# Kernel tuning notes

Hardware: AMD Instinct MI355X
Metric: run time of the kernel (lower is better)

The kernel has to match this reference:

```python
import jax, jax.numpy as jnp
import numpy as np

RCUT, RCUT_SMTH = 6.0, 0.5
SEL = [32, 64]
SEC = [0, 32, 96]
PAIRS = [(0, 0), (0, 1), (1, 1)]  # (ti, tj) with ti <= tj, matching stacked weight index
NF, NLOC, NALL = 1, 256, 512
NNEI = sum(SEL)
NG = 96


def setup_inputs() -> dict:
    key = jax.random.key(0)
    ks = jax.random.split(key, 10)
    # coords in a 4A cube so most neighbor distances are inside rcut=6
    extended_coord = jax.random.uniform(ks[0], (NF, NALL * 3), dtype=jnp.float32) * 4.0
    nl = jax.random.randint(ks[1], (NF, NLOC, NNEI), 0, NALL - 1)
    # shift indices >= own local index by 1 to avoid self-neighbors (zero distance)
    nlist = nl + (nl >= jnp.arange(NLOC)[None, :, None]).astype(nl.dtype)
    extended_atype = jax.random.randint(ks[2], (NF, NALL), 0, 2)
    mean = jnp.zeros((2, NNEI, 4), jnp.float32)
    stddev = jnp.ones((2, NNEI, 4), jnp.float32)
    def w(k, shape, fan):
        return jax.random.normal(k, shape, jnp.float32) / np.float32(np.sqrt(fan))
    W1 = w(ks[3], (3, 1, 24), 1.0)
    b1 = 0.1 * jax.random.normal(ks[4], (3, 24), jnp.float32)
    W2 = w(ks[5], (3, 24, 48), 24.0)
    b2 = 0.1 * jax.random.normal(ks[6], (3, 48), jnp.float32)
    W3 = w(ks[7], (3, 48, 96), 48.0)
    b3 = 0.1 * jax.random.normal(ks[8], (3, 96), jnp.float32)
    return dict(nlist=nlist, extended_coord=extended_coord, extended_atype=extended_atype,
                mean=mean, stddev=stddev, W1=W1, b1=b1, W2=W2, b2=b2, W3=W3, b3=b3)


def _smooth_weight(r, rmin, rmax):
    uu = (r - rmin) / (rmax - rmin)
    vv = uu * uu * uu * (-6.0 * uu * uu + 15.0 * uu - 10.0) + 1.0
    return jnp.where(r <= rmin, 1.0, jnp.where(r >= rmax, 0.0, vv))


def _env_mat(nlist, coord, atype, mean, stddev):
    nf, nloc, nnei = nlist.shape
    coord = coord.reshape(nf, -1, 3)
    mask = nlist >= 0
    nl = jnp.where(mask, nlist, 0)
    # gather neighbor coords: nf x nloc x nnei x 3
    coord_r = jnp.take_along_axis(coord, nl.reshape(nf, -1, 1), axis=1).reshape(nf, nloc, nnei, 3)
    diff = coord_r - coord[:, :nloc, None, :]
    length = jnp.linalg.norm(diff, axis=-1, keepdims=True)
    length = length + (~mask)[..., None].astype(diff.dtype)  # avoid 0-div on padded entries
    t0 = 1.0 / length
    t1 = diff / (length * length)
    sw = _smooth_weight(length, RCUT_SMTH, RCUT) * mask[..., None].astype(diff.dtype)
    env = jnp.concatenate([t0, t1], axis=-1) * sw  # nf x nloc x nnei x 4
    loc_type = atype[:, :nloc]
    dmatrix = (env - mean[loc_type]) / stddev[loc_type]
    return dmatrix, sw


def _embed(x, W1, b1, W2, b2, W3, b3):
    # EmbeddingNet 1->24->48->96, tanh, resnet doubling residuals
    h1 = jnp.tanh(x @ W1 + b1)
    h2 = jnp.tanh(h1 @ W2 + b2) + jnp.concatenate([h1, h1], axis=-1)
    h3 = jnp.tanh(h2 @ W3 + b3) + jnp.concatenate([h2, h2], axis=-1)
    return h3


def reference(nlist, extended_coord, extended_atype, mean, stddev, W1, b1, W2, b2, W3, b3):
    nf, nloc, nnei = nlist.shape
    dmatrix, sw = _env_mat(nlist, extended_coord, extended_atype, mean, stddev)
    dm = dmatrix.reshape(nf * nloc, nnei, 4)
    result = jnp.zeros((nf * nloc, NG), dm.dtype)
    for p, (ti, tj) in enumerate(PAIRS):
        rr_i = dm[:, SEC[ti]:SEC[ti + 1], 1:]  # nfnl x nt_i x 3
        rr_j = dm[:, SEC[tj]:SEC[tj + 1], 1:]  # nfnl x nt_j x 3
        env_ij = jnp.einsum('ijm,ikm->ijk', rr_i, rr_j)  # nfnl x nt_i x nt_j
        gg = _embed(env_ij[..., None], W1[p], b1[p], W2[p], b2[p], W3[p], b3[p])
        res_ij = jnp.einsum('ijk,ijkm->im', env_ij, gg)
        result = result + res_ij * (1.0 / (SEL[ti] * SEL[tj]))
    return result.reshape(nf, nloc, NG)
```

## Files before the change

kernel.cpp:

```cpp
#include <hip/hip_runtime.h>

#define NLOC 256
#define NNEI 96
#define NG   96
#define S2LE 2.88539008177793f

typedef __attribute__((ext_vector_type(8))) short short8;
typedef __attribute__((ext_vector_type(4))) float f32x4;
union Frag { uint4 u; short8 s; };

__device__ __forceinline__ float tanh_sc(float s) {
    float e = __builtin_amdgcn_exp2f(s);
    return 1.0f - 2.0f * __builtin_amdgcn_rcpf(e + 1.0f);
}
__device__ __forceinline__ unsigned short f2bf(float f) {
    unsigned int u = __float_as_uint(f);
    u += 0x7FFFu + ((u >> 16) & 1u);
    return (unsigned short)(u >> 16);
}
__device__ __forceinline__ unsigned short f2bf_rhu(float f) {
    return (unsigned short)((__float_as_uint(f) + 0x8000u) >> 16);
}
__device__ __forceinline__ unsigned int pack_bf2(float lo, float hi) {
    unsigned int a = __float_as_uint(lo) + 0x8000u;
    unsigned int b = __float_as_uint(hi) + 0x8000u;
    return __builtin_amdgcn_perm(b, a, 0x07060302);
}
__device__ __forceinline__ void wave_fence() {
    asm volatile("s_waitcnt lgkmcnt(0)" ::: "memory");
    __builtin_amdgcn_sched_barrier(0);
}

__global__ __launch_bounds__(256) void prep_kernel(
        const float* __restrict__ W1, const float* __restrict__ b1,
        const float* __restrict__ W2, const float* __restrict__ b2,
        const float* __restrict__ W3, const float* __restrict__ b3,
        unsigned short* __restrict__ wf2, unsigned short* __restrict__ wf3,
        unsigned short* __restrict__ wfJ,
        float* __restrict__ w1s, float* __restrict__ b1s,
        float* __restrict__ b2s, float* __restrict__ b3s,
        const int* __restrict__ nlist, const float* __restrict__ coord,
        const int* __restrict__ atype,
        const float* __restrict__ mean, const float* __restrict__ stddev,
        float4* __restrict__ rrle) {
    if (blockIdx.x >= 15) {
        if (rrle == nullptr) return;
        int t = (blockIdx.x - 15) * 256 + threadIdx.x;
        int i = t / 96, n = t - i * 96;
        int idx = nlist[i * NNEI + n];
        bool msk = idx >= 0;
        int safe = msk ? idx : 0;
        float cx = coord[i*3], cy = coord[i*3+1], cz = coord[i*3+2];
        float dx = coord[safe*3]   - cx;
        float dy = coord[safe*3+1] - cy;
        float dz = coord[safe*3+2] - cz;
        float rn = sqrtf(dx*dx + dy*dy + dz*dz) + (msk ? 0.0f : 1.0f);
        float sw;
        if (rn <= 0.5f)      sw = 1.0f;
        else if (rn >= 6.0f) sw = 0.0f;
        else {
            float uu = (rn - 0.5f) * (1.0f / 5.5f);
            sw = uu*uu*uu*(uu*(-6.0f*uu + 15.0f) - 10.0f) + 1.0f;
        }
        if (!msk) sw = 0.0f;
        float ir2 = 1.0f / (rn * rn);
        int ty = atype[i];
        const float* mu = mean   + (ty * NNEI + n) * 4;
        const float* sd = stddev + (ty * NNEI + n) * 4;
        float vx = (dx * ir2 * sw - mu[1]) / sd[1];
        float vy = (dy * ir2 * sw - mu[2]) / sd[2];
        float vz = (dz * ir2 * sw - mu[3]) / sd[3];
        rrle[t] = make_float4(vx, vy, vz, 0.0f);
        return;
    }
    int t = blockIdx.x * blockDim.x + threadIdx.x;
    if (t < 2880) {
        int p = t / 960;
        int r = t % 960;
        int tile = r / 64;
        int l = r % 64;
        int nlo = l & 15, g = l >> 4;
        short8 v;
        if (tile < 3) {
            int nt = tile;
            #pragma unroll
            for (int j = 0; j < 8; j++) {
                int k = g * 8 + j;
                float w = (k < 24) ? W2[(p * 24 + k) * 48 + nt * 16 + nlo] * S2LE : 0.0f;
                v[j] = (short)f2bf(w);
            }
            *(short8*)(wf2 + ((p * 3 + nt) * 64 + l) * 8) = v;
        } else {
            int tt = tile - 3;
            int nt = tt >> 1, kc = tt & 1;
            #pragma unroll
            for (int j = 0; j < 8; j++) {
                int kk = (kc == 0) ? (g * 8 + j) : ((j < 4) ? (32 + g * 4 + j) : -1);
                float w = (kk >= 0) ? W3[(p * 48 + kk) * 96 + nt * 16 + nlo] * S2LE : 0.0f;
                v[j] = (short)f2bf(w);
            }
            *(short8*)(wf3 + ((p * 12 + nt * 2 + kc) * 64 + l) * 8) = v;
        }
    } else if (t < 3264) {
        int t2 = t - 2880;
        int f = t2 >> 6, l = t2 & 63;
        int ml = l & 15, g = l >> 4;
        short8 v;
        if (f < 3) {
            int c24 = (f * 16 + ml) % 24;
            #pragma unroll
            for (int j = 0; j < 8; j++)
                v[j] = (short)((g * 8 + j == c24) ? 0x3F80 : 0);
        } else {
            int nt2 = f - 3;
            if (nt2 < 2) {
                int c = nt2 * 16 + ml;
                #pragma unroll
                for (int j = 0; j < 8; j++)
                    v[j] = (short)((g * 8 + j == c) ? 0x3F80 : 0);
            } else {
                #pragma unroll
                for (int j = 0; j < 8; j++)
                    v[j] = (short)((j < 4 && (g * 4 + j) == ml) ? 0x3F80 : 0);
            }
        }
        *(short8*)(wfJ + (f * 64 + l) * 8) = v;
    } else if (t < 3768) {
        int u = t - 3264;
        if (u < 72)       { w1s[u] = W1[u] * S2LE; b1s[u] = b1[u] * S2LE; }
        else if (u < 216) { b2s[u - 72]  = b2[u - 72]  * S2LE; }
        else              { b3s[u - 216] = b3[u - 216] * S2LE; }
    }
}

template<bool GR>
__launch_bounds__(256)
__global__ void mlp_kernel(const int* __restrict__ nlist, const float* __restrict__ coord,
                           const int* __restrict__ atype,
                           const float* __restrict__ mean, const float* __restrict__ stddev,
                           const float* __restrict__ w1s, const float* __restrict__ b1s,
                           const float* __restrict__ b2s, const float* __restrict__ b3s,
                           const unsigned short* __restrict__ wf2,
                           const unsigned short* __restrict__ wf3,
                           const unsigned short* __restrict__ wfJ,
                           const float4* __restrict__ rrle,
                           float* __restrict__ out) {
    __shared__ __align__(16) unsigned char smem[40448];
    unsigned short* h1s = (unsigned short*)smem;
    unsigned short* h2s = (unsigned short*)(smem + 12288);
    float*          resf = (float*)(smem + 38912);
    unsigned char*  h2b = smem + 12288;

    int tid = threadIdx.x;
    int blk = blockIdx.x;
    int i = blk / 20;
    int b = blk - i * 20;

    int p, base_e, offi, offj, count, Aint;
    float scale;
    bool tri;
    if (b < 3)       { p=0; base_e=b*256;      offi=0;  offj=0;  scale=1.0f/1024.0f; count=528;  tri=true;  Aint=65;  }
    else if (b < 11) { p=1; base_e=(b-3)*256;  offi=0;  offj=32; scale=1.0f/2048.0f; count=2048; tri=false; Aint=0;   }
    else             { p=2; base_e=(b-11)*256; offi=32; offj=32; scale=1.0f/4096.0f; count=2080; tri=true;  Aint=129; }

    int l  = tid & 63;
    int w  = tid >> 6;
    int ml = l & 15, g = l >> 4;

    if (!GR) {
        if (tid < NNEI) {
            int n = tid;
            int idx = nlist[i * NNEI + n];
            bool msk = idx >= 0;
            int safe = msk ? idx : 0;
            float cx = coord[i*3], cy = coord[i*3+1], cz = coord[i*3+2];
            float dx = coord[safe*3]   - cx;
            float dy = coord[safe*3+1] - cy;
            float dz = coord[safe*3+2] - cz;
            float rn = sqrtf(dx*dx + dy*dy + dz*dz) + (msk ? 0.0f : 1.0f);
            float sw;
            if (rn <= 0.5f)      sw = 1.0f;
            else if (rn >= 6.0f) sw = 0.0f;
            else {
                float uu = (rn - 0.5f) * (1.0f / 5.5f);
                sw = uu*uu*uu*(uu*(-6.0f*uu + 15.0f) - 10.0f) + 1.0f;
            }
            if (!msk) sw = 0.0f;
            float ir2 = 1.0f / (rn * rn);
            int ty = atype[i];
            const float* mu = mean   + (ty * NNEI + n) * 4;
            const float* sd = stddev + (ty * NNEI + n) * 4;
            float vx = (dx * ir2 * sw - mu[1]) / sd[1];
            float vy = (dy * ir2 * sw - mu[2]) / sd[2];
            float vz = (dz * ir2 * sw - mu[3]) / sd[3];
            float* hp = (float*)(h2b + (96 + n) * 104 + 96);
            hp[0] = vx; hp[1] = vy;
            *(float*)(h2b + (192 + (n >> 1)) * 104 + 96 + ((n & 1) << 2)) = vz;
        }
        __syncthreads();
    }

    float xs;
    {
        int e = base_e + tid;
        bool valid = e < count;
        int ec = valid ? e : 0;
        int jj, kk;
        float mult = 1.0f;
        if (!tri) { jj = ec >> 6; kk = ec & 63; }
        else {
            float Af = (float)Aint;
            int j = (int)((Af - sqrtf(Af*Af - 8.0f*(float)ec)) * 0.5f);
            int Tj1 = ((j+1)*(Aint-j-1)) >> 1;
            if (ec >= Tj1) j++;
            int Tj = (j*(Aint-j)) >> 1;
            if (ec < Tj) { j--; Tj = (j*(Aint-j)) >> 1; }
            jj = j; kk = j + (ec - Tj);
            mult = (jj == kk) ? 1.0f : 2.0f;
        }
        int ja = offi + jj, kb = offj + kk;
        float x;
        if (GR) {
            float4 ra = rrle[i * NNEI + ja];
            float4 rb = rrle[i * NNEI + kb];
            x = ra.x*rb.x + ra.y*rb.y + ra.z*rb.z;
        } else {
            const float* pa = (const float*)(h2b + (96 + ja) * 104 + 96);
            const float* pb = (const float*)(h2b + (96 + kb) * 104 + 96);
            float az = *(const float*)(h2b + (192 + (ja >> 1)) * 104 + 96 + ((ja & 1) << 2));
            float bz = *(const float*)(h2b + (192 + (kb >> 1)) * 104 + 96 + ((kb & 1) << 2));
            x = pa[0]*pb[0] + pa[1]*pb[1] + az*bz;
        }
        x = valid ? x : 0.0f;
        xs = x * mult * scale;

        const float* w1 = w1s + p * 24;
        const float* c1 = b1s + p * 24;
        float h1v[24];
        #pragma unroll
        for (int u = 0; u < 24; u++)
            h1v[u] = tanh_sc(fmaf(x, w1[u], c1[u]));
        #pragma unroll
        for (int t8 = 0; t8 < 3; t8++) {
            uint4 q = make_uint4(pack_bf2(h1v[8*t8+0], h1v[8*t8+1]),
                                 pack_bf2(h1v[8*t8+2], h1v[8*t8+3]),
                                 pack_bf2(h1v[8*t8+4], h1v[8*t8+5]),
                                 pack_bf2(h1v[8*t8+6], h1v[8*t8+7]));
            *(uint4*)(h1s + tid*24 + 8*t8) = q;
        }
    }
    wave_fence();

    short8 bw2[3], jf2[3];
    float  b2c[3];
    #pragma unroll
    for (int nt = 0; nt < 3; nt++) {
        bw2[nt] = *(const short8*)(wf2 + ((p*3 + nt)*64 + l)*8);
        jf2[nt] = *(const short8*)(wfJ + (nt*64 + l)*8);
        b2c[nt] = b2s[p*48 + nt*16 + ml];
    }
    f32x4 ones = {1.f, 1.f, 1.f, 1.f};
    int aoff = (g == 3) ? 0 : g * 8;
    #pragma unroll
    for (int mi = 0; mi < 4; mi++) {
        int mt = w*4 + mi;
        int arow = mt*16 + ml;
        uint2 lo = *(const uint2*)(h1s + arow*24 + aoff);
        uint2 hi = *(const uint2*)(h1s + arow*24 + aoff + 4);
        Frag fa; fa.u = make_uint4(lo.x, lo.y, hi.x, hi.y);
        #pragma unroll
        for (int nt = 0; nt < 3; nt++) {
            f32x4 bini = {b2c[nt], b2c[nt], b2c[nt], b2c[nt]};
            f32x4 acc = __builtin_amdgcn_mfma_f32_16x16x32_bf16(fa.s, bw2[nt], bini, 0, 0, 0);
            f32x4 aj  = __builtin_amdgcn_mfma_f32_16x16x32_bf16(fa.s, jf2[nt], ones, 0, 0, 0);
            int col = nt*16 + ml;
            #pragma unroll
            for (int r = 0; r < 4; r++) {
                int orow = mt*16 + g*4 + r;
                float e2 = __builtin_amdgcn_exp2f(acc[r]);
                float rc = __builtin_amdgcn_rcpf(e2 + 1.0f);
                float v  = fmaf(-2.0f, rc, aj[r]);
                h2s[orow*52 + col] = f2bf_rhu(v);
            }
        }
    }
    wave_fence();

    short8 a3a[4], a3b[4];
    float  xv[4][4];
    #pragma unroll
    for (int mi = 0; mi < 4; mi++) {
        int mt = w*4 + mi;
        int arow = mt*16 + ml;
        uint2 lo = *(const uint2*)(h2s + arow*52 + g*8);
        uint2 hi = *(const uint2*)(h2s + arow*52 + g*8 + 4);
        Frag fa; fa.u = make_uint4(lo.x, lo.y, hi.x, hi.y);
        a3a[mi] = fa.s;
        uint2 t2 = *(const uint2*)(h2s + arow*52 + 32 + g*4);
        Frag fb; fb.u = make_uint4(t2.x, t2.y, 0u, 0u);
        a3b[mi] = fb.s;
        int xb = (l & 48) + mi * 64;
        #pragma unroll
        for (int r = 0; r < 4; r++)
            xv[mi][r] = __int_as_float(
                __builtin_amdgcn_ds_bpermute(xb + r*4, __float_as_int(xs)));
    }
    short8 jf3[3];
    #pragma unroll
    for (int q = 0; q < 3; q++)
        jf3[q] = *(const short8*)(wfJ + ((3 + q)*64 + l)*8);

    #pragma unroll
    for (int nt2 = 0; nt2 < 3; nt2++) {
        f32x4 ajp[4];
        #pragma unroll
        for (int mi = 0; mi < 4; mi++)
            ajp[mi] = __builtin_amdgcn_mfma_f32_16x16x32_bf16(
                (nt2 == 2) ? a3b[mi] : a3a[mi], jf3[nt2], ones, 0, 0, 0);
        #pragma unroll
        for (int h = 0; h < 2; h++) {
            int nt = nt2 + 3*h;
            short8 b30 = *(const short8*)(wf3 + ((p*12 + nt*2 + 0)*64 + l)*8);
            short8 b31 = *(const short8*)(wf3 + ((p*12 + nt*2 + 1)*64 + l)*8);
            float b3c = b3s[p*96 + nt*16 + ml];
            float facc = 0.0f;
            #pragma unroll
            for (int mi = 0; mi < 4; mi++) {
                f32x4 bini = {b3c, b3c, b3c, b3c};
                f32x4 acc = __builtin_amdgcn_mfma_f32_16x16x32_bf16(a3a[mi], b30, bini, 0, 0, 0);
                acc = __builtin_amdgcn_mfma_f32_16x16x32_bf16(a3b[mi], b31, acc, 0, 0, 0);
                #pragma unroll
                for (int r = 0; r < 4; r++) {
                    float e2 = __builtin_amdgcn_exp2f(acc[r]);
                    float rc = __builtin_amdgcn_rcpf(e2 + 1.0f);
                    float h3 = fmaf(-2.0f, rc, ajp[mi][r]);
                    facc = fmaf(xv[mi][r], h3, facc);
                }
            }
            facc += __shfl_xor(facc, 16, 64);
            facc += __shfl_xor(facc, 32, 64);
            if (l < 16) resf[w*96 + nt*16 + ml] = facc;
        }
    }
    __syncthreads();
    if (tid < NG) {
        float s = resf[tid] + resf[96 + tid] + resf[192 + tid] + resf[288 + tid];
        atomicAdd(&out[i*NG + tid], s);
    }
}

extern "C" void kernel_launch(void* const* d_in, const int* in_sizes, int n_in,
                              void* d_out, int out_size, void* d_ws, size_t ws_size,
                              hipStream_t stream) {
    const int*   nlist  = (const int*)  d_in[0];
    const float* coord  = (const float*)d_in[1];
    const int*   atype  = (const int*)  d_in[2];
    const float* mean   = (const float*)d_in[3];
    const float* stddev = (const float*)d_in[4];
    const float* W1     = (const float*)d_in[5];
    const float* b1     = (const float*)d_in[6];
    const float* W2     = (const float*)d_in[7];
    const float* b2     = (const float*)d_in[8];
    const float* W3     = (const float*)d_in[9];
    const float* b3     = (const float*)d_in[10];
    float* out = (float*)d_out;

    char* ws = (char*)d_ws;
    unsigned short* wf2 = (unsigned short*)(ws + 0);
    unsigned short* wf3 = (unsigned short*)(ws + 9216);
    unsigned short* wfJ = (unsigned short*)(ws + 46080);
    float* w1s = (float*)(ws + 52224);
    float* b1s = (float*)(ws + 52512);
    float* b2s = (float*)(ws + 52800);
    float* b3s = (float*)(ws + 53376);
    size_t need = 55296 + (size_t)NLOC * NNEI * 16;
    bool gr = ws_size >= need;
    float4* rrle = gr ? (float4*)(ws + 55296) : nullptr;

    prep_kernel<<<gr ? 111 : 15, 256, 0, stream>>>(
        W1, b1, W2, b2, W3, b3, wf2, wf3, wfJ, w1s, b1s, b2s, b3s,
        nlist, coord, atype, mean, stddev, rrle);
    if (gr)
        mlp_kernel<true><<<NLOC * 20, 256, 0, stream>>>(
            nlist, coord, atype, mean, stddev,
            w1s, b1s, b2s, b3s, wf2, wf3, wfJ, rrle, out);
    else
        mlp_kernel<false><<<NLOC * 20, 256, 0, stream>>>(
            nlist, coord, atype, mean, stddev,
            w1s, b1s, b2s, b3s, wf2, wf3, wfJ, rrle, out);
}
```

Measured before the change: 135.2 us.

## Process layer-2/3 in two row chunks to shrink shared memory footprint

Splits each wave's four M-tiles into two chunks of two, computing the layer-2 output into a smaller per-chunk shared buffer and consuming it immediately in layer 3 while accumulating partial sums in registers. This cuts LDS usage per block from about 40KB to 27KB so more blocks can be resident per CU, and reduces live fragment registers. The env-matrix staging moves into the result buffer, which needs an extra block barrier in the non-GR path. The cost is more loop overhead, more wave fences and an extra sync.

```diff
diff --git a/kernel.cpp b/kernel.cpp
--- a/kernel.cpp
+++ b/kernel.cpp
@@ -145,11 +145,11 @@
                            const unsigned short* __restrict__ wfJ,
                            const float4* __restrict__ rrle,
                            float* __restrict__ out) {
-    __shared__ __align__(16) unsigned char smem[40448];
-    unsigned short* h1s = (unsigned short*)smem;
-    unsigned short* h2s = (unsigned short*)(smem + 12288);
-    float*          resf = (float*)(smem + 38912);
-    unsigned char*  h2b = smem + 12288;
+    __shared__ __align__(16) unsigned char smem[27136];
+    unsigned short* h1s  = (unsigned short*)smem;
+    unsigned char*  h1b  = smem;
+    unsigned char*  h2c  = smem + 12288;
+    float*          resf = (float*)(smem + 25600);
 
     int tid = threadIdx.x;
     int blk = blockIdx.x;
@@ -190,12 +190,9 @@
             int ty = atype[i];
             const float* mu = mean   + (ty * NNEI + n) * 4;
             const float* sd = stddev + (ty * NNEI + n) * 4;
-            float vx = (dx * ir2 * sw - mu[1]) / sd[1];
-            float vy = (dy * ir2 * sw - mu[2]) / sd[2];
-            float vz = (dz * ir2 * sw - mu[3]) / sd[3];
-            float* hp = (float*)(h2b + (96 + n) * 104 + 96);
-            hp[0] = vx; hp[1] = vy;
-            *(float*)(h2b + (192 + (n >> 1)) * 104 + 96 + ((n & 1) << 2)) = vz;
+            resf[n*3+0] = (dx * ir2 * sw - mu[1]) / sd[1];
+            resf[n*3+1] = (dy * ir2 * sw - mu[2]) / sd[2];
+            resf[n*3+2] = (dz * ir2 * sw - mu[3]) / sd[3];
         }
         __syncthreads();
     }
@@ -225,11 +222,8 @@
             float4 rb = rrle[i * NNEI + kb];
             x = ra.x*rb.x + ra.y*rb.y + ra.z*rb.z;
         } else {
-            const float* pa = (const float*)(h2b + (96 + ja) * 104 + 96);
-            const float* pb = (const float*)(h2b + (96 + kb) * 104 + 96);
-            float az = *(const float*)(h2b + (192 + (ja >> 1)) * 104 + 96 + ((ja & 1) << 2));
-            float bz = *(const float*)(h2b + (192 + (kb >> 1)) * 104 + 96 + ((kb & 1) << 2));
-            x = pa[0]*pb[0] + pa[1]*pb[1] + az*bz;
+            x = resf[ja*3+0]*resf[kb*3+0] + resf[ja*3+1]*resf[kb*3+1]
+              + resf[ja*3+2]*resf[kb*3+2];
         }
         x = valid ? x : 0.0f;
         xs = x * mult * scale;
@@ -246,101 +240,117 @@
                                  pack_bf2(h1v[8*t8+2], h1v[8*t8+3]),
                                  pack_bf2(h1v[8*t8+4], h1v[8*t8+5]),
                                  pack_bf2(h1v[8*t8+6], h1v[8*t8+7]));
-            *(uint4*)(h1s + tid*24 + 8*t8) = q;
+            *(uint4*)(h1b + tid*48 + 16*t8) = q;
         }
     }
     wave_fence();
-
-    short8 bw2[3], jf2[3];
-    float  b2c[3];
+    if (!GR) __syncthreads();
+
+    short8 bw2[3], jf2[3], jf3[3];
+    float  b2c[3], b3c6[6];
     #pragma unroll
     for (int nt = 0; nt < 3; nt++) {
         bw2[nt] = *(const short8*)(wf2 + ((p*3 + nt)*64 + l)*8);
         jf2[nt] = *(const short8*)(wfJ + (nt*64 + l)*8);
+        jf3[nt] = *(const short8*)(wfJ + ((3 + nt)*64 + l)*8);
         b2c[nt] = b2s[p*48 + nt*16 + ml];
     }
+    #pragma unroll
+    for (int q = 0; q < 6; q++) {
+        int nt = (q >> 1) + 3 * (q & 1);
+        b3c6[q] = b3s[p*96 + nt*16 + ml];
+    }
     f32x4 ones = {1.f, 1.f, 1.f, 1.f};
-    int aoff = (g == 3) ? 0 : g * 8;
+    int aoffB = (g == 3) ? 0 : g * 16;
+    float facc[6] = {0.f, 0.f, 0.f, 0.f, 0.f, 0.f};
+
     #pragma unroll
-    for (int mi = 0; mi < 4; mi++) {
-        int mt = w*4 + mi;
-        int arow = mt*16 + ml;
-        uint2 lo = *(const uint2*)(h1s + arow*24 + aoff);
-        uint2 hi = *(const uint2*)(h1s + arow*24 + aoff + 4);
-        Frag fa; fa.u = make_uint4(lo.x, lo.y, hi.x, hi.y);
+    for (int c = 0; c < 2; c++) {
         #pragma unroll
-        for (int nt = 0; nt < 3; nt++) {
-            f32x4 bini = {b2c[nt], b2c[nt], b2c[nt], b2c[nt]};
-            f32x4 acc = __builtin_amdgcn_mfma_f32_16x16x32_bf16(fa.s, bw2[nt], bini, 0, 0, 0);
-            f32x4 aj  = __builtin_amdgcn_mfma_f32_16x16x32_bf16(fa.s, jf2[nt], ones, 0, 0, 0);
-            int col = nt*16 + ml;
-            #pragma unroll
-            for (int r = 0; r < 4; r++) {
-                int orow = mt*16 + g*4 + r;
-                float e2 = __builtin_amdgcn_exp2f(acc[r]);
-                float rc = __builtin_amdgcn_rcpf(e2 + 1.0f);
-                float v  = fmaf(-2.0f, rc, aj[r]);
-                h2s[orow*52 + col] = f2bf_rhu(v);
-            }
-        }
-    }
-    wave_fence();
-
-    short8 a3a[4], a3b[4];
-    float  xv[4][4];
-    #pragma unroll
-    for (int mi = 0; mi < 4; mi++) {
-        int mt = w*4 + mi;
-        int arow = mt*16 + ml;
-        uint2 lo = *(const uint2*)(h2s + arow*52 + g*8);
-        uint2 hi = *(const uint2*)(h2s + arow*52 + g*8 + 4);
-        Frag fa; fa.u = make_uint4(lo.x, lo.y, hi.x, hi.y);
-        a3a[mi] = fa.s;
-        uint2 t2 = *(const uint2*)(h2s + arow*52 + 32 + g*4);
-        Frag fb; fb.u = make_uint4(t2.x, t2.y, 0u, 0u);
-        a3b[mi] = fb.s;
-        int xb = (l & 48) + mi * 64;
-        #pragma unroll
-        for (int r = 0; r < 4; r++)
-            xv[mi][r] = __int_as_float(
-                __builtin_amdgcn_ds_bpermute(xb + r*4, __float_as_int(xs)));
-    }
-    short8 jf3[3];
-    #pragma unroll
-    for (int q = 0; q < 3; q++)
-        jf3[q] = *(const short8*)(wfJ + ((3 + q)*64 + l)*8);
-
-    #pragma unroll
-    for (int nt2 = 0; nt2 < 3; nt2++) {
-        f32x4 ajp[4];
-        #pragma unroll
-        for (int mi = 0; mi < 4; mi++)
-            ajp[mi] = __builtin_amdgcn_mfma_f32_16x16x32_bf16(
-                (nt2 == 2) ? a3b[mi] : a3a[mi], jf3[nt2], ones, 0, 0, 0);
-        #pragma unroll
-        for (int h = 0; h < 2; h++) {
-            int nt = nt2 + 3*h;
-            short8 b30 = *(const short8*)(wf3 + ((p*12 + nt*2 + 0)*64 + l)*8);
-            short8 b31 = *(const short8*)(wf3 + ((p*12 + nt*2 + 1)*64 + l)*8);
-            float b3c = b3s[p*96 + nt*16 + ml];
-            float facc = 0.0f;
-            #pragma unroll
-            for (int mi = 0; mi < 4; mi++) {
-                f32x4 bini = {b3c, b3c, b3c, b3c};
-                f32x4 acc = __builtin_amdgcn_mfma_f32_16x16x32_bf16(a3a[mi], b30, bini, 0, 0, 0);
-                acc = __builtin_amdgcn_mfma_f32_16x16x32_bf16(a3b[mi], b31, acc, 0, 0, 0);
+        for (int m01 = 0; m01 < 2; m01++) {
+            int mi2 = c*2 + m01;
+            int mt = w*4 + mi2;
+            int arow = mt*16 + ml;
+            uint2 lo = *(const uint2*)(h1b + arow*48 + aoffB);
+            uint2 hi = *(const uint2*)(h1b + arow*48 + aoffB + 8);
+            Frag fa; fa.u = make_uint4(lo.x, lo.y, hi.x, hi.y);
+            int lbase = w*32 + m01*16 + g*4;
+            #pragma unroll
+            for (int nt = 0; nt < 3; nt++) {
+                f32x4 bini = {b2c[nt], b2c[nt], b2c[nt], b2c[nt]};
+                f32x4 acc = __builtin_amdgcn_mfma_f32_16x16x32_bf16(fa.s, bw2[nt], bini, 0, 0, 0);
+                f32x4 aj  = __builtin_amdgcn_mfma_f32_16x16x32_bf16(fa.s, jf2[nt], ones, 0, 0, 0);
+                int col = nt*16 + ml;
                 #pragma unroll
                 for (int r = 0; r < 4; r++) {
                     float e2 = __builtin_amdgcn_exp2f(acc[r]);
                     float rc = __builtin_amdgcn_rcpf(e2 + 1.0f);
-                    float h3 = fmaf(-2.0f, rc, ajp[mi][r]);
-                    facc = fmaf(xv[mi][r], h3, facc);
+                    float v  = fmaf(-2.0f, rc, aj[r]);
+                    *(unsigned short*)(h2c + (lbase + r)*104 + col*2) = f2bf_rhu(v);
                 }
             }
-            facc += __shfl_xor(facc, 16, 64);
-            facc += __shfl_xor(facc, 32, 64);
-            if (l < 16) resf[w*96 + nt*16 + ml] = facc;
-        }
+        }
+        wave_fence();
+
+        short8 a3a[2], a3b[2];
+        float  xv[2][4];
+        #pragma unroll
+        for (int m01 = 0; m01 < 2; m01++) {
+            int mi2 = c*2 + m01;
+            int lrow = w*32 + m01*16 + ml;
+            uint2 lo = *(const uint2*)(h2c + lrow*104 + g*16);
+            uint2 hi = *(const uint2*)(h2c + lrow*104 + g*16 + 8);
+            Frag fa; fa.u = make_uint4(lo.x, lo.y, hi.x, hi.y);
+            a3a[m01] = fa.s;
+            uint2 t2 = *(const uint2*)(h2c + lrow*104 + 64 + g*8);
+            Frag fb; fb.u = make_uint4(t2.x, t2.y, 0u, 0u);
+            a3b[m01] = fb.s;
+            int xb = (l & 48) + mi2 * 64;
+            #pragma unroll
+            for (int r = 0; r < 4; r++)
+                xv[m01][r] = __int_as_float(
+                    __builtin_amdgcn_ds_bpermute(xb + r*4, __float_as_int(xs)));
+        }
+        #pragma unroll
+        for (int nt2 = 0; nt2 < 3; nt2++) {
+            f32x4 ajp[2];
+            #pragma unroll
+            for (int m01 = 0; m01 < 2; m01++)
+                ajp[m01] = __builtin_amdgcn_mfma_f32_16x16x32_bf16(
+                    (nt2 == 2) ? a3b[m01] : a3a[m01], jf3[nt2], ones, 0, 0, 0);
+            #pragma unroll
+            for (int h = 0; h < 2; h++) {
+                int nt = nt2 + 3*h;
+                short8 b30 = *(const short8*)(wf3 + ((p*12 + nt*2 + 0)*64 + l)*8);
+                short8 b31 = *(const short8*)(wf3 + ((p*12 + nt*2 + 1)*64 + l)*8);
+                float b3c = b3c6[nt2*2 + h];
+                float fsum = facc[nt2*2 + h];
+                #pragma unroll
+                for (int m01 = 0; m01 < 2; m01++) {
+                    f32x4 bini = {b3c, b3c, b3c, b3c};
+                    f32x4 acc = __builtin_amdgcn_mfma_f32_16x16x32_bf16(a3a[m01], b30, bini, 0, 0, 0);
+                    acc = __builtin_amdgcn_mfma_f32_16x16x32_bf16(a3b[m01], b31, acc, 0, 0, 0);
+                    #pragma unroll
+                    for (int r = 0; r < 4; r++) {
+                        float e2 = __builtin_amdgcn_exp2f(acc[r]);
+                        float rc = __builtin_amdgcn_rcpf(e2 + 1.0f);
+                        float h3 = fmaf(-2.0f, rc, ajp[m01][r]);
+                        fsum = fmaf(xv[m01][r], h3, fsum);
+                    }
+                }
+                facc[nt2*2 + h] = fsum;
+            }
+        }
+        wave_fence();
+    }
+
+    #pragma unroll
+    for (int q = 0; q < 6; q++) {
+        int nt = (q >> 1) + 3 * (q & 1);
+        float f = facc[q];
+        f += __shfl_xor(f, 16, 64);
+        f += __shfl_xor(f, 32, 64);
+        if (l < 16) resf[w*96 + nt*16 + ml] = f;
     }
     __syncthreads();
     if (tid < NG) {
```

New measurement: 149.4 us. +10.5%, slower.
